# Kernel tuning notes

Hardware: AMD Instinct MI355X
Metric: run time of the kernel (lower is better)

The kernel has to match this reference:

```python
import math
import jax, jax.numpy as jnp
import numpy as np

F0_BINS = 64; FRAME_HOP = 240; SR = 48000; LO_DIM = 16; N_HARM = 32
NOISE_FFT = 256; N_NOISE = NOISE_FFT // 2 + 1; VEL_DIM = 8
F0_MAX = 5000.0; F0_MIN = 20.0
B, T = 4, 500
NSAMP = T * FRAME_HOP
MLP, HID = 128, 64
FEAT = F0_BINS + LO_DIM + VEL_DIM  # 88


def _sincos_enc(norm, dim):
    # norm: (...,) in [0,1] -> (..., dim), even slots sin, odd slots cos
    i = jnp.arange(1, dim // 2 + 1, dtype=jnp.float32)
    ang = math.pi * i * norm[..., None]                    # (..., dim/2)
    return jnp.stack([jnp.sin(ang), jnp.cos(ang)], axis=-1).reshape(norm.shape + (dim,))


def lin_interp(x, out_len):
    # matches F.interpolate(mode='linear', align_corners=False); x: (..., Tin)
    Tin = x.shape[-1]
    pos = jnp.clip((jnp.arange(out_len, dtype=jnp.float32) + 0.5) * (Tin / out_len) - 0.5, 0.0, Tin - 1.0)
    i0 = jnp.floor(pos).astype(jnp.int32)
    i1 = jnp.minimum(i0 + 1, Tin - 1)
    w = pos - i0
    return x[..., i0] * (1.0 - w) + x[..., i1] * w


def _hann(n):
    return 0.5 - 0.5 * jnp.cos(2.0 * math.pi * jnp.arange(n, dtype=jnp.float32) / n)


def _stft(x, n_fft, hop, window):
    # torch.stft with center=True (reflect pad); returns (B, n_fft//2+1, n_frames)
    pad = n_fft // 2
    xp = jnp.pad(x, ((0, 0), (pad, pad)), mode='reflect')
    n_frames = 1 + (xp.shape[-1] - n_fft) // hop
    idx = jnp.arange(n_frames)[:, None] * hop + jnp.arange(n_fft)[None, :]
    frames = xp[:, idx] * window                           # (B, F, n_fft)
    return jnp.swapaxes(jnp.fft.rfft(frames, axis=-1), 1, 2)


def _istft(spec, n_fft, hop, window, length):
    frames = jnp.fft.irfft(jnp.swapaxes(spec, 1, 2), n=n_fft, axis=-1) * window  # (B, F, n_fft)
    nF = frames.shape[1]
    out_len = n_fft + hop * (nF - 1)
    idx = jnp.arange(nF)[:, None] * hop + jnp.arange(n_fft)[None, :]
    ola = jnp.zeros((frames.shape[0], out_len), frames.dtype).at[:, idx].add(frames)
    wsum = jnp.zeros((out_len,), frames.dtype).at[idx].add(jnp.broadcast_to(window ** 2, idx.shape))
    ola = ola / jnp.maximum(wsum, 1e-11)
    pad = n_fft // 2
    return ola[:, pad:pad + length]


def _gru(x, W_ih, W_hh, b_ih, b_hh):
    # torch nn.GRU, 1 layer, batch_first; gates ordered (r, z, n)
    H = W_hh.shape[1]
    def step(h, xt):
        gi = xt @ W_ih.T + b_ih
        gh = h @ W_hh.T + b_hh
        ir, iz, inn = jnp.split(gi, 3, axis=-1)
        hr, hz, hn = jnp.split(gh, 3, axis=-1)
        r = jax.nn.sigmoid(ir + hr)
        z = jax.nn.sigmoid(iz + hz)
        n = jnp.tanh(inn + r * hn)
        h_new = (1.0 - z) * n + z * h
        return h_new, h_new
    h0 = jnp.zeros((x.shape[0], H), x.dtype)
    _, ys = jax.lax.scan(step, h0, jnp.swapaxes(x, 0, 1))
    return jnp.swapaxes(ys, 0, 1)


def _harm_synth(harm_amps, overall_amp, f0_hz, n_samples):
    Bn, Tf, N = harm_amps.shape
    a = lin_interp(jnp.swapaxes(harm_amps, 1, 2), n_samples)      # (B, N, n)
    oa = lin_interp(jnp.swapaxes(overall_amp, 1, 2), n_samples)   # (B, 1, n)
    f0_up = lin_interp(f0_hz, n_samples)                          # (B, n)
    k = jnp.arange(1, N + 1, dtype=jnp.float32)
    inst_freq = f0_up[:, None, :] * k[None, :, None]              # (B, N, n)
    a = a * (inst_freq < SR * 0.45).astype(a.dtype)
    mean_freq = inst_freq.mean(axis=2, keepdims=True)             # (B, N, 1) -- faithful to source
    t = jnp.arange(n_samples, dtype=jnp.float32)
    phase = (2.0 * math.pi / SR) * mean_freq * t[None, None, :]
    return (a * jnp.sin(phase)).sum(axis=1, keepdims=True) * oa   # (B, 1, n)


def _noise_synth(noise_mags, noise, n_samples, n_fft=NOISE_FFT):
    hop = n_fft // 4
    window = _hann(n_fft)
    spec = _stft(noise, n_fft, hop, window)                       # (B, 129, T_stft)
    T_stft = spec.shape[-1]
    mag = lin_interp(jnp.swapaxes(noise_mags, 1, 2), T_stft)      # (B, 129, T_stft)
    return _istft(spec * mag, n_fft, hop, window, n_samples)[:, None, :]


def setup_inputs() -> dict:
    key = jax.random.key(0)
    ks = jax.random.split(key, 20)
    def lin(k, o, i, s=0.05):
        return jax.random.normal(k, (o, i), dtype=jnp.float32) * s
    inp = {
        'f0_hz': jax.random.uniform(ks[0], (B, T), jnp.float32) * 1980.0 + 20.0,
        'loudness_db': jax.random.uniform(ks[1], (B, T), jnp.float32) * -80.0,
        'velocity': jax.random.uniform(ks[2], (B,), jnp.float32) * 7.0,
        'noise_L': jax.random.normal(ks[3], (B, NSAMP), jnp.float32),
        'noise_R': jax.random.normal(ks[4], (B, NSAMP), jnp.float32),
        'W_pre1': lin(ks[5], MLP, FEAT), 'b_pre1': jnp.zeros((MLP,), jnp.float32),
        'W_pre2': lin(ks[6], MLP, MLP), 'b_pre2': jnp.zeros((MLP,), jnp.float32),
        'W_ih': lin(ks[7], 3 * HID, MLP), 'W_hh': lin(ks[8], 3 * HID, HID),
        'b_ih': jnp.zeros((3 * HID,), jnp.float32), 'b_hh': jnp.zeros((3 * HID,), jnp.float32),
        'W_post': lin(ks[9], MLP, HID), 'b_post': jnp.zeros((MLP,), jnp.float32),
        'W_hL': lin(ks[10], N_HARM, MLP), 'b_hL': jnp.zeros((N_HARM,), jnp.float32),
        'W_hR': lin(ks[11], N_HARM, MLP), 'b_hR': jnp.zeros((N_HARM,), jnp.float32),
        'W_amp': lin(ks[12], 1, MLP), 'b_amp': jnp.zeros((1,), jnp.float32),
        'W_nL': lin(ks[13], N_NOISE, MLP), 'b_nL': jnp.full((N_NOISE,), -3.0, jnp.float32),
        'W_nR': lin(ks[14], N_NOISE, MLP), 'b_nR': jnp.full((N_NOISE,), -3.0, jnp.float32),
    }
    return inp


def reference(f0_hz, loudness_db, velocity, noise_L, noise_R,
              W_pre1, b_pre1, W_pre2, b_pre2,
              W_ih, W_hh, b_ih, b_hh, W_post, b_post,
              W_hL, b_hL, W_hR, b_hR, W_amp, b_amp,
              W_nL, b_nL, W_nR, b_nR):
    Bn, Tn = f0_hz.shape
    # --- sinusoidal encodings ---
    f0_safe = jnp.clip(f0_hz, F0_MIN, None)
    f0_norm = jnp.clip((jnp.log(f0_safe) - math.log(F0_MIN)) / (math.log(F0_MAX) - math.log(F0_MIN)), 0.0, 1.0)
    f0_enc = _sincos_enc(f0_norm, F0_BINS) * (f0_hz > 0).astype(jnp.float32)[..., None]
    lo_enc = _sincos_enc(jnp.clip((loudness_db + 80.0) / 80.0, 0.0, 1.0), LO_DIM)
    vel_enc = _sincos_enc(jnp.clip(velocity / 7.0, 0.0, 1.0), VEL_DIM)  # (B, VEL_DIM)
    vel_enc = jnp.broadcast_to(vel_enc[:, None, :], (Bn, Tn, VEL_DIM))
    feat = jnp.concatenate([f0_enc, lo_enc, vel_enc], axis=-1)          # (B, T, 88)
    # --- trunk ---
    feat = jax.nn.relu(feat @ W_pre1.T + b_pre1)
    feat = jax.nn.relu(feat @ W_pre2.T + b_pre2)
    feat = _gru(feat, W_ih, W_hh, b_ih, b_hh)
    feat = jax.nn.relu(feat @ W_post.T + b_post)
    # --- heads ---
    harm_L = jax.nn.sigmoid(feat @ W_hL.T + b_hL)
    harm_R = jax.nn.sigmoid(feat @ W_hR.T + b_hR)
    overall_amp = jax.nn.softplus(feat @ W_amp.T + b_amp)               # (B, T, 1)
    nmag_L = jax.nn.sigmoid(feat @ W_nL.T + b_nL)
    nmag_R = jax.nn.sigmoid(feat @ W_nR.T + b_nR)
    n_samples = Tn * FRAME_HOP
    # --- synthesis ---
    L = _harm_synth(harm_L, overall_amp, f0_hz, n_samples) + _noise_synth(nmag_L, noise_L, n_samples)
    R = _harm_synth(harm_R, overall_amp, f0_hz, n_samples) + _noise_synth(nmag_R, noise_R, n_samples)
    return jnp.concatenate([L, R], axis=1)                              # (B, 2, n_samples)
```

## Files before the change

### kernel.cpp

```cpp
#include <hip/hip_runtime.h>
#include <math.h>

#ifndef M_PI
#define M_PI 3.14159265358979323846
#endif

#define BB 4
#define TT 500
#define NSAMP 120000
#define NHARM 32
#define NFFT 256
#define NBIN 129
#define NHOPF 64
#define NFRAMES 1876
#define HID 64
#define MLPD 128
#define FEATD 88

#define R_MAG ((float)(500.0/1876.0))
#define R_UP_F ((float)(500.0/120000.0))

#define OFF_HARML 0
#define OFF_HARMR 64000
#define OFF_AMP   128000
#define OFF_NMAGL 130000
#define OFF_NMAGR 388000
#define OFF_C1    646000
#define OFF_H1    646128
#define OFF_GI    (OFF_H1+256000)
#define OFF_GOUT  (OFF_GI+384000)
#define OFF_SPECL (OFF_GOUT+128000)
#define OFF_SPECR (OFF_SPECL+4*NFRAMES*258)

__device__ __forceinline__ void up_coords(int m, int* i0, int* i1, float* w, float* w1){
  float pos = __fadd_rn(__fmul_rn(__fadd_rn((float)m, 0.5f), R_UP_F), -0.5f);
  pos = fminf(fmaxf(pos, 0.0f), 499.0f);
  int a = (int)pos;
  *i0 = a; *i1 = min(a+1, TT-1);
  float ww = __fsub_rn(pos, (float)a);
  *w = ww; *w1 = __fsub_rn(1.0f, ww);
}
__device__ __forceinline__ float f0_up_elem(const float* __restrict__ f0s, int m){
  int i0,i1; float w,w1;
  up_coords(m,&i0,&i1,&w,&w1);
  return __fadd_rn(__fmul_rn(f0s[i0], w1), __fmul_rn(f0s[i1], w));
}

__global__ __launch_bounds__(128) void k_encmm(const float* __restrict__ f0,
    const float* __restrict__ ldb, const float* __restrict__ vel,
    const float* __restrict__ Wp1, const float* __restrict__ bp1,
    float* __restrict__ h1){
  int row = blockIdx.x;
  int b = row / TT;
  int tid = threadIdx.x;
  __shared__ float feat[FEATD];
  if (tid < FEATD){
    float f = f0[row];
    float gate = (f > 0.0f) ? 1.0f : 0.0f;
    float fs = fmaxf(f, 20.0f);
    float fn = (logf(fs) - (float)2.995732273553991) / (float)5.5214609178622464;
    fn = fminf(fmaxf(fn, 0.0f), 1.0f);
    float ln = fminf(fmaxf((ldb[row] + 80.0f) / 80.0f, 0.0f), 1.0f);
    float vn = fminf(fmaxf(vel[b] / 7.0f, 0.0f), 1.0f);
    float norm; int i; float g2 = 1.0f;
    if (tid < 64){ i = (tid>>1) + 1; norm = fn; g2 = gate; }
    else if (tid < 80){ i = ((tid-64)>>1) + 1; norm = ln; }
    else { i = ((tid-80)>>1) + 1; norm = vn; }
    float ang = (float)M_PI * (float)i * norm;
    feat[tid] = ((tid & 1) ? cosf(ang) : sinf(ang)) * g2;
  }
  __syncthreads();
  const float* wp = Wp1 + tid*FEATD;
  float acc = bp1[tid];
  #pragma unroll 8
  for (int i=0;i<FEATD;i++) acc = fmaf(feat[i], wp[i], acc);
  h1[(size_t)row*MLPD + tid] = fmaxf(acc, 0.0f);
}

__global__ __launch_bounds__(192) void k_mm2gi(const float* __restrict__ h1,
    const float* __restrict__ Wp2, const float* __restrict__ bp2,
    const float* __restrict__ Wih, const float* __restrict__ bih,
    float* __restrict__ gi){
  int row = blockIdx.x;
  int tid = threadIdx.x;
  __shared__ float h1s[MLPD];
  __shared__ float h2s[MLPD];
  if (tid < MLPD) h1s[tid] = h1[(size_t)row*MLPD + tid];
  __syncthreads();
  if (tid < MLPD){
    const float* wp = Wp2 + tid*MLPD;
    float acc = bp2[tid];
    #pragma unroll 8
    for (int i=0;i<MLPD;i++) acc = fmaf(h1s[i], wp[i], acc);
    h2s[tid] = fmaxf(acc, 0.0f);
  }
  __syncthreads();
  const float* wp = Wih + tid*MLPD;
  float acc = bih[tid];
  #pragma unroll 8
  for (int i=0;i<MLPD;i++) acc = fmaf(h2s[i], wp[i], acc);
  gi[(size_t)row*192 + tid] = acc;
}

__device__ float np_block_sum(const float* __restrict__ f0s, int off, int n, float kf){
  float r[8];
  #pragma unroll
  for (int j=0;j<8;j++) r[j] = __fmul_rn(f0_up_elem(f0s, off+j), kf);
  int lim = n - (n & 7);
  int i = 8;
  for (; i<lim; i+=8){
    #pragma unroll
    for (int j=0;j<8;j++)
      r[j] = __fadd_rn(r[j], __fmul_rn(f0_up_elem(f0s, off+i+j), kf));
  }
  float res = __fadd_rn(__fadd_rn(__fadd_rn(r[0],r[1]), __fadd_rn(r[2],r[3])),
                        __fadd_rn(__fadd_rn(r[4],r[5]), __fadd_rn(r[6],r[7])));
  for (; i<n; i++)
    res = __fadd_rn(res, __fmul_rn(f0_up_elem(f0s, off+i), kf));
  return res;
}

#define MID_GRU   BB
#define MID_MF    (MID_GRU + BB*32)
#define STFT_JOBS (2*BB*NFRAMES)
#define MID_STFT_BLOCKS ((STFT_JOBS+5)/6)
#define MID_BLOCKS (MID_MF + MID_STFT_BLOCKS)

#define RL(x,l) __uint_as_float(__builtin_amdgcn_readlane(__float_as_uint(x), (l)))

#define CH  25
#define NCH 20

__device__ __forceinline__ float fsig(float x){
  return __fdividef(1.0f, 1.0f + __expf(-x));
}
__device__ __forceinline__ float ftanh(float x){
  return fmaf(-2.0f, __fdividef(1.0f, 1.0f + __expf(2.0f*x)), 1.0f);
}

__global__ __launch_bounds__(384) void k_mid(
    const float* __restrict__ gi, const float* __restrict__ Whh,
    const float* __restrict__ bhh, float* __restrict__ gout,
    const float* __restrict__ f0, const float* __restrict__ nL,
    const float* __restrict__ nR, float* __restrict__ ws){
  __shared__ __align__(16) float sh[13696];
  int blk = blockIdx.x;
  int tid = threadIdx.x;

  if (blk < MID_GRU){
    float* gibuf = sh;
    float* hist  = sh + 9600;
    int b = blk;
    int j = tid & 63;
    float wr[64], wz[64], wn[64];
    float br=0.f, bz=0.f, bn=0.f;
    if (tid < 64){
      #pragma unroll
      for (int i=0;i<16;i++){
        float4 a = *(const float4*)(Whh + (size_t)(j)*64     + i*4);
        float4 c = *(const float4*)(Whh + (size_t)(64+j)*64  + i*4);
        float4 d = *(const float4*)(Whh + (size_t)(128+j)*64 + i*4);
        wr[4*i]=a.x; wr[4*i+1]=a.y; wr[4*i+2]=a.z; wr[4*i+3]=a.w;
        wz[4*i]=c.x; wz[4*i+1]=c.y; wz[4*i+2]=c.z; wz[4*i+3]=c.w;
        wn[4*i]=d.x; wn[4*i+1]=d.y; wn[4*i+2]=d.z; wn[4*i+3]=d.w;
      }
      br = bhh[j]; bz = bhh[64+j]; bn = bhh[128+j];
    }
    const float* gbase = gi + (size_t)b*TT*192;
    if (tid >= 64){
      int pt = tid - 64;
      for (int idx = pt; idx < CH*48; idx += 192){
        float4 v = *(const float4*)(gbase + idx*4);
        *(float4*)&gibuf[idx*4] = v;
      }
    }
    __syncthreads();
    float hreg = 0.0f;
    float* op = gout + (size_t)b*TT*64;
    for (int c=0; c<NCH; c++){
      if (tid >= 64){
        if (c+1 < NCH){
          int pt = tid - 64;
          const float* src = gbase + (size_t)(c+1)*CH*192;
          float* dst = &gibuf[((c+1)&1)*4800];
          for (int idx = pt; idx < CH*48; idx += 192){
            float4 v = *(const float4*)(src + idx*4);
            *(float4*)&dst[idx*4] = v;
          }
        }
      } else {
        const float* gch = &gibuf[(c&1)*4800];
        for (int tt=0; tt<CH; tt++){
          int t = c*CH + tt;
          float gr0 = gch[tt*192 + j];
          float gz0 = gch[tt*192 + 64 + j];
          float gn0 = gch[tt*192 + 128 + j];
          float ar0=0.f,ar1=0.f,ar2=0.f,ar3=0.f;
          float az0=0.f,az1=0.f,az2=0.f,az3=0.f;
          float an0=0.f,an1=0.f,an2=0.f,an3=0.f;
          #pragma unroll
          for (int i=0;i<16;i++){
            float h0 = RL(hreg, i), h1v = RL(hreg, 16+i);
            float h2v = RL(hreg, 32+i), h3v = RL(hreg, 48+i);
            ar0 = fmaf(wr[i],    h0,  ar0); ar1 = fmaf(wr[16+i], h1v, ar1);
            ar2 = fmaf(wr[32+i], h2v, ar2); ar3 = fmaf(wr[48+i], h3v, ar3);
            az0 = fmaf(wz[i],    h0,  az0); az1 = fmaf(wz[16+i], h1v, az1);
            az2 = fmaf(wz[32+i], h2v, az2); az3 = fmaf(wz[48+i], h3v, az3);
            an0 = fmaf(wn[i],    h0,  an0); an1 = fmaf(wn[16+i], h1v, an1);
            an2 = fmaf(wn[32+i], h2v, an2); an3 = fmaf(wn[48+i], h3v, an3);
          }
          float ar = __fadd_rn(__fadd_rn(ar0,ar1), __fadd_rn(ar2,ar3));
          float az = __fadd_rn(__fadd_rn(az0,az1), __fadd_rn(az2,az3));
          float an = __fadd_rn(__fadd_rn(an0,an1), __fadd_rn(an2,an3));
          float r = fsig(gr0 + ar + br);
          float z = fsig(gz0 + az + bz);
          float n = ftanh(gn0 + r*(an+bn));
          hreg = (1.0f - z)*n + z*hreg;
          int th = t & 63;
          hist[th*64 + j] = hreg;
          if (th == 63 || t == TT-1){
            int base_t = t - th;
            int per = th + 1;
            int nb = per >> 2;
            float* dst2 = op + base_t*64 + j*per;
            for (int q=0;q<nb;q++){
              float4 v = *(float4*)&hist[j*per + q*4];
              *(float4*)&dst2[q*4] = v;
            }
          }
        }
      }
      __syncthreads();
    }
  } else if (blk < MID_MF){
    int bk = blk - MID_GRU;
    int b = bk >> 5, k = bk & 31;
    float kf = (float)(k+1);
    float* f0s = sh;
    float* red = sh + 512;
    for (int i=tid;i<TT;i+=384) f0s[i] = f0[b*TT+i];
    __syncthreads();
    if (tid < 256){
      float lv[4];
      #pragma unroll
      for (int q=0;q<4;q++){
        int leafIdx = tid*4 + q;
        int off = 0, n = NSAMP;
        #pragma unroll
        for (int lvl=9; lvl>=0; --lvl){
          int n2 = (n>>1); n2 -= (n2 & 7);
          if ((leafIdx >> lvl) & 1){ off += n2; n -= n2; } else { n = n2; }
        }
        lv[q] = np_block_sum(f0s, off, n, kf);
      }
      red[tid] = __fadd_rn(__fadd_rn(lv[0],lv[1]), __fadd_rn(lv[2],lv[3]));
    }
    __syncthreads();
    for (int cnt=256; cnt>1; cnt>>=1){
      int half = cnt>>1;
      float v = 0.0f;
      if (tid < half) v = __fadd_rn(red[2*tid], red[2*tid+1]);
      __syncthreads();
      if (tid < half) red[tid] = v;
      __syncthreads();
    }
    if (tid==0){
      float mf = __fdiv_rn(red[0], 120000.0f);
      float c1 = __fmul_rn((float)(2.0*M_PI/48000.0), mf);
      ws[OFF_C1 + b*32 + k] = c1;
    }
  } else {
    int base = (blk - MID_MF)*6;
    int sub = tid >> 6;
    int j = tid & 63;
    float2* tw = (float2*)sh;
    float* frs = sh + 512 + sub*256;
    if (tid < 256){
      double a = (2.0*M_PI/256.0)*(double)tid;
      tw[tid] = make_float2((float)cos(a), (float)sin(a));
    }
    int jid = base + sub;
    bool act = jid < STFT_JOBS;
    int b=0, f=0; const float* x = nL;
    if (act){
      int ch = jid / (BB*NFRAMES);
      int rem = jid - ch*(BB*NFRAMES);
      b = rem / NFRAMES; f = rem - b*NFRAMES;
      x = (ch ? nR : nL) + (size_t)b*NSAMP;
      for (int n=j;n<256;n+=64){
        double a = (2.0*M_PI/256.0)*(double)n;
        int xi = f*NHOPF + n - 128;
        xi = xi < 0 ? -xi : xi;
        xi = xi >= NSAMP ? 2*(NSAMP-1)-xi : xi;
        float wnd = (float)(0.5 - 0.5*cos(a));
        frs[n] = x[xi]*wnd;
      }
    }
    __syncthreads();
    if (act){
      int ch = jid / (BB*NFRAMES);
      float* spec = ws + (ch ? OFF_SPECR : OFF_SPECL) + (size_t)(b*NFRAMES+f)*258;
      float re0=0.f, im0=0.f, re1=0.f, im1=0.f;
      int m0 = 0;
      #pragma unroll 4
      for (int n=0;n<256;n++){
        float fv = frs[n];
        int m1 = (m0 + ((n&3)<<6)) & 255;
        float2 t0 = tw[m0], t1 = tw[m1];
        re0 = fmaf(fv, t0.x, re0); im0 = fmaf(-fv, t0.y, im0);
        re1 = fmaf(fv, t1.x, re1); im1 = fmaf(-fv, t1.y, im1);
        m0 = (m0 + j) & 255;
      }
      float pq = frs[j] + frs[j+64] + frs[j+128] + frs[j+192];
      pq = (j & 1) ? -pq : pq;
      for (int o2=32;o2>0;o2>>=1) pq += __shfl_down(pq, o2, 64);
      spec[2*j]   = re0; spec[2*j+1]   = im0;
      spec[2*(j+64)] = re1; spec[2*(j+64)+1] = im1;
      if (j==0){ spec[256] = pq; spec[257] = 0.0f; }
    }
  }
}

__global__ __launch_bounds__(128) void k_posthead(const float* __restrict__ gout,
  const float* __restrict__ Wpo, const float* __restrict__ bpo,
  const float* __restrict__ WhL, const float* __restrict__ bhL,
  const float* __restrict__ WhR, const float* __restrict__ bhR,
  const float* __restrict__ Wam, const float* __restrict__ bam,
  const float* __restrict__ WnL, const float* __restrict__ bnL,
  const float* __restrict__ WnR, const float* __restrict__ bnR,
  float* __restrict__ harmL, float* __restrict__ harmR, float* __restrict__ amp,
  float* __restrict__ nmagL, float* __restrict__ nmagR){
  int row = blockIdx.x;
  int tid = threadIdx.x;
  __shared__ float gs[HID];
  __shared__ float post[MLPD];
  if (tid < HID) gs[tid] = gout[(size_t)row*HID + tid];
  __syncthreads();
  {
    const float* wp = Wpo + tid*HID;
    float acc = bpo[tid];
    #pragma unroll 8
    for (int i=0;i<HID;i++) acc = fmaf(gs[i], wp[i], acc);
    post[tid] = fmaxf(acc, 0.0f);
  }
  __syncthreads();
  #pragma unroll
  for (int rr=0;rr<3;rr++){
    int c = tid + rr*128;
    if (c >= 323) break;
    const float* W; const float* bb; float* o; int oc, ow; bool sp=false;
    if (c < 32)      { W=WhL; bb=bhL; o=harmL; oc=c;     ow=32; }
    else if (c < 64) { W=WhR; bb=bhR; o=harmR; oc=c-32;  ow=32; }
    else if (c == 64){ W=Wam; bb=bam; o=amp;   oc=0;     ow=1; sp=true; }
    else if (c < 194){ W=WnL; bb=bnL; o=nmagL; oc=c-65;  ow=129; }
    else             { W=WnR; bb=bnR; o=nmagR; oc=c-194; ow=129; }
    const float* wp = W + oc*MLPD;
    float acc = bb[oc];
    #pragma unroll 8
    for (int i=0;i<MLPD;i++) acc = fmaf(post[i], wp[i], acc);
    float v;
    if (sp) v = fmaxf(acc, 0.0f) + log1pf(expf(-fabsf(acc)));
    else    v = 1.0f/(1.0f+expf(-acc));
    o[(size_t)row*ow + oc] = v;
  }
}

__global__ __launch_bounds__(256) void k_istft(float* __restrict__ ws){
  int fr = blockIdx.x;
  int ch = blockIdx.y;
  int b = fr / NFRAMES, f = fr - b*NFRAMES;
  float* spec = ws + (ch ? OFF_SPECR : OFF_SPECL) + (size_t)fr*258;
  const float* nmag = ws + (ch ? OFF_NMAGR : OFF_NMAGL) + (size_t)b*TT*NBIN;
  int t = threadIdx.x;
  __shared__ float2 mx[NBIN];
  double a = (2.0*M_PI/256.0)*(double)t;
  float cz = (float)cos(a), sz = (float)sin(a);
  if (t < NBIN){
    float pos = ((float)f + 0.5f) * R_MAG - 0.5f;
    pos = fminf(fmaxf(pos, 0.0f), 499.0f);
    int i0 = (int)pos, i1 = min(i0+1, TT-1);
    float w = pos - (float)i0;
    float mg = nmag[i0*NBIN + t]*(1.0f-w) + nmag[i1*NBIN + t]*w;
    mx[t] = make_float2(spec[2*t]*mg, spec[2*t+1]*mg);
  }
  __syncthreads();
  float acc0 = mx[0].x + ((t&1) ? -mx[128].x : mx[128].x);
  float acc = 0.0f;
  float c = cz, s = sz;
  #pragma unroll 4
  for (int k=1;k<128;k++){
    float2 v = mx[k];
    acc = fmaf(v.x, c, acc);
    acc = fmaf(-v.y, s, acc);
    float ts_ = s*sz, tc_ = c*sz;
    float cn = fmaf(c, cz, -ts_);
    float sn = fmaf(s, cz,  tc_);
    c = cn; s = sn;
  }
  float y = (acc0 + 2.0f*acc) * (1.0f/256.0f);
  float win = 0.5f - 0.5f*cz;
  spec[t] = y*win;
}

__global__ __launch_bounds__(256) void k_out(const float* __restrict__ f0,
    const float* __restrict__ ws, float* __restrict__ out){
  __shared__ float win2[256];
  __shared__ float c1s[BB*32];
  {
    int t = threadIdx.x;
    double a = (2.0*M_PI/256.0)*(double)t;
    float w = (float)(0.5 - 0.5*cos(a));
    win2[t] = w*w;
    if (t < BB*32) c1s[t] = ws[OFF_C1 + t];
  }
  __syncthreads();
  int idx = blockIdx.x*256 + threadIdx.x;
  if (idx >= BB*2*NSAMP) return;
  int m = idx % NSAMP;
  int bc = idx / NSAMP;
  int ch = bc & 1, b = bc >> 1;
  int i0,i1; float w,w1;
  up_coords(m,&i0,&i1,&w,&w1);
  const float* f0b = f0 + b*TT;
  float f0u = __fadd_rn(__fmul_rn(f0b[i0], w1), __fmul_rn(f0b[i1], w));
  const float* am = ws + OFF_AMP + b*TT;
  float oa = __fadd_rn(__fmul_rn(am[i0], w1), __fmul_rn(am[i1], w));
  const float* ha = ws + (ch ? OFF_HARMR : OFF_HARML) + (size_t)b*TT*NHARM;
  float tm = (float)m;
  float hsum = 0.0f;
  for (int k=1;k<=NHARM;k++){
    float instf = __fmul_rn(f0u, (float)k);
    if (instf < 21600.0f){
      float a0 = ha[i0*NHARM + (k-1)], a1 = ha[i1*NHARM + (k-1)];
      float ak = __fadd_rn(__fmul_rn(a0, w1), __fmul_rn(a1, w));
      float ph = __fmul_rn(c1s[b*32 + (k-1)], tm);
      double rev = (double)ph * 0.15915494309189535;
      double fr2 = rev - floor(rev);
      float rad = (float)((fr2 - (fr2 >= 0.5 ? 1.0 : 0.0)) * 6.283185307179586);
      float s = sinf(rad);
      hsum = __fadd_rn(hsum, __fmul_rn(ak, s));
    }
  }
  float harm = __fmul_rn(hsum, oa);
  int p = m + 128;
  int fhi = min(p >> 6, NFRAMES-1);
  int flo = max((p - 192) >> 6, 0);
  const float* frb = ws + (ch ? OFF_SPECR : OFF_SPECL) + (size_t)b*NFRAMES*258;
  float nacc = 0.0f, wsum = 0.0f;
  for (int f=flo; f<=fhi; f++){
    int n = p - f*NHOPF;
    nacc += frb[f*258 + n];
    wsum += win2[n];
  }
  float noise = nacc / fmaxf(wsum, 1e-11f);
  out[idx] = __fadd_rn(harm, noise);
}

extern "C" void kernel_launch(void* const* d_in, const int* in_sizes, int n_in,
                              void* d_out, int out_size, void* d_ws, size_t ws_size,
                              hipStream_t stream){
  const float* f0  = (const float*)d_in[0];
  const float* ldb = (const float*)d_in[1];
  const float* vel = (const float*)d_in[2];
  const float* nL  = (const float*)d_in[3];
  const float* nR  = (const float*)d_in[4];
  const float* Wp1 = (const float*)d_in[5];
  const float* bp1 = (const float*)d_in[6];
  const float* Wp2 = (const float*)d_in[7];
  const float* bp2 = (const float*)d_in[8];
  const float* Wih = (const float*)d_in[9];
  const float* Whh = (const float*)d_in[10];
  const float* bih = (const float*)d_in[11];
  const float* bhh = (const float*)d_in[12];
  const float* Wpo = (const float*)d_in[13];
  const float* bpo = (const float*)d_in[14];
  const float* WhL = (const float*)d_in[15];
  const float* bhL = (const float*)d_in[16];
  const float* WhR = (const float*)d_in[17];
  const float* bhR = (const float*)d_in[18];
  const float* Wam = (const float*)d_in[19];
  const float* bam = (const float*)d_in[20];
  const float* WnL = (const float*)d_in[21];
  const float* bnL = (const float*)d_in[22];
  const float* WnR = (const float*)d_in[23];
  const float* bnR = (const float*)d_in[24];
  float* ws = (float*)d_ws;
  float* out = (float*)d_out;

  k_encmm<<<BB*TT, 128, 0, stream>>>(f0, ldb, vel, Wp1, bp1, ws+OFF_H1);
  k_mm2gi<<<BB*TT, 192, 0, stream>>>(ws+OFF_H1, Wp2, bp2, Wih, bih, ws+OFF_GI);
  k_mid<<<MID_BLOCKS, 384, 0, stream>>>(ws+OFF_GI, Whh, bhh, ws+OFF_GOUT, f0, nL, nR, ws);
  k_posthead<<<BB*TT, 128, 0, stream>>>(ws+OFF_GOUT, Wpo, bpo,
      WhL,bhL, WhR,bhR, Wam,bam, WnL,bnL, WnR,bnR,
      ws+OFF_HARML, ws+OFF_HARMR, ws+OFF_AMP, ws+OFF_NMAGL, ws+OFF_NMAGR);
  dim3 gs(BB*NFRAMES, 2);
  k_istft<<<gs, 256, 0, stream>>>(ws);
  k_out<<<(BB*2*NSAMP+255)/256, 256, 0, stream>>>(f0, ws, out);
}
```

Measured before the change: 457.0 us.

## Fuse front MLP kernels and use packed FMA in GRU recurrence

Merges the encoder/first-layer kernel with the second-layer/GRU-input kernel, so h1 stays in shared memory and one launch plus a global round trip are removed. In the serial GRU recurrence inside k_mid, the 64-wide dot products are rewritten with two-element vector FMAs, which can map to packed FP32 FMA on CDNA3-class hardware and halve the FMA issue count on the critical serial path. k_mid also gets an explicit waves-per-EU hint to steer register allocation. The packed form changes the summation order slightly, and the occupancy hint may affect the other roles that share k_mid.

```diff
diff --git a/kernel.cpp b/kernel.cpp
--- a/kernel.cpp
+++ b/kernel.cpp
@@ -20,6 +20,8 @@
 #define R_MAG ((float)(500.0/1876.0))
 #define R_UP_F ((float)(500.0/120000.0))
 
+typedef float v2f __attribute__((ext_vector_type(2)));
+
 #define OFF_HARML 0
 #define OFF_HARMR 64000
 #define OFF_AMP   128000
@@ -46,14 +48,18 @@
   return __fadd_rn(__fmul_rn(f0s[i0], w1), __fmul_rn(f0s[i1], w));
 }
 
-__global__ __launch_bounds__(128) void k_encmm(const float* __restrict__ f0,
+__global__ __launch_bounds__(192) void k_front(const float* __restrict__ f0,
     const float* __restrict__ ldb, const float* __restrict__ vel,
     const float* __restrict__ Wp1, const float* __restrict__ bp1,
-    float* __restrict__ h1){
+    const float* __restrict__ Wp2, const float* __restrict__ bp2,
+    const float* __restrict__ Wih, const float* __restrict__ bih,
+    float* __restrict__ gi){
   int row = blockIdx.x;
   int b = row / TT;
   int tid = threadIdx.x;
   __shared__ float feat[FEATD];
+  __shared__ float h1s[MLPD];
+  __shared__ float h2s[MLPD];
   if (tid < FEATD){
     float f = f0[row];
     float gate = (f > 0.0f) ? 1.0f : 0.0f;
@@ -70,22 +76,13 @@
     feat[tid] = ((tid & 1) ? cosf(ang) : sinf(ang)) * g2;
   }
   __syncthreads();
-  const float* wp = Wp1 + tid*FEATD;
-  float acc = bp1[tid];
-  #pragma unroll 8
-  for (int i=0;i<FEATD;i++) acc = fmaf(feat[i], wp[i], acc);
-  h1[(size_t)row*MLPD + tid] = fmaxf(acc, 0.0f);
-}
-
-__global__ __launch_bounds__(192) void k_mm2gi(const float* __restrict__ h1,
-    const float* __restrict__ Wp2, const float* __restrict__ bp2,
-    const float* __restrict__ Wih, const float* __restrict__ bih,
-    float* __restrict__ gi){
-  int row = blockIdx.x;
-  int tid = threadIdx.x;
-  __shared__ float h1s[MLPD];
-  __shared__ float h2s[MLPD];
-  if (tid < MLPD) h1s[tid] = h1[(size_t)row*MLPD + tid];
+  if (tid < MLPD){
+    const float* wp = Wp1 + tid*FEATD;
+    float acc = bp1[tid];
+    #pragma unroll 8
+    for (int i=0;i<FEATD;i++) acc = fmaf(feat[i], wp[i], acc);
+    h1s[tid] = fmaxf(acc, 0.0f);
+  }
   __syncthreads();
   if (tid < MLPD){
     const float* wp = Wp2 + tid*MLPD;
@@ -95,11 +92,13 @@
     h2s[tid] = fmaxf(acc, 0.0f);
   }
   __syncthreads();
-  const float* wp = Wih + tid*MLPD;
-  float acc = bih[tid];
-  #pragma unroll 8
-  for (int i=0;i<MLPD;i++) acc = fmaf(h2s[i], wp[i], acc);
-  gi[(size_t)row*192 + tid] = acc;
+  {
+    const float* wp = Wih + tid*MLPD;
+    float acc = bih[tid];
+    #pragma unroll 8
+    for (int i=0;i<MLPD;i++) acc = fmaf(h2s[i], wp[i], acc);
+    gi[(size_t)row*192 + tid] = acc;
+  }
 }
 
 __device__ float np_block_sum(const float* __restrict__ f0s, int off, int n, float kf){
@@ -138,7 +137,10 @@
   return fmaf(-2.0f, __fdividef(1.0f, 1.0f + __expf(2.0f*x)), 1.0f);
 }
 
-__global__ __launch_bounds__(384) void k_mid(
+__global__
+__attribute__((amdgpu_flat_work_group_size(384,384)))
+__attribute__((amdgpu_waves_per_eu(2,2)))
+void k_mid(
     const float* __restrict__ gi, const float* __restrict__ Whh,
     const float* __restrict__ bhh, float* __restrict__ gout,
     const float* __restrict__ f0, const float* __restrict__ nL,
@@ -152,7 +154,7 @@
     float* hist  = sh + 9600;
     int b = blk;
     int j = tid & 63;
-    float wr[64], wz[64], wn[64];
+    v2f wr2[32], wz2[32], wn2[32];
     float br=0.f, bz=0.f, bn=0.f;
     if (tid < 64){
       #pragma unroll
@@ -160,9 +162,9 @@
         float4 a = *(const float4*)(Whh + (size_t)(j)*64     + i*4);
         float4 c = *(const float4*)(Whh + (size_t)(64+j)*64  + i*4);
         float4 d = *(const float4*)(Whh + (size_t)(128+j)*64 + i*4);
-        wr[4*i]=a.x; wr[4*i+1]=a.y; wr[4*i+2]=a.z; wr[4*i+3]=a.w;
-        wz[4*i]=c.x; wz[4*i+1]=c.y; wz[4*i+2]=c.z; wz[4*i+3]=c.w;
-        wn[4*i]=d.x; wn[4*i+1]=d.y; wn[4*i+2]=d.z; wn[4*i+3]=d.w;
+        wr2[2*i] = (v2f){a.x, a.y}; wr2[2*i+1] = (v2f){a.z, a.w};
+        wz2[2*i] = (v2f){c.x, c.y}; wz2[2*i+1] = (v2f){c.z, c.w};
+        wn2[2*i] = (v2f){d.x, d.y}; wn2[2*i+1] = (v2f){d.z, d.w};
       }
       br = bhh[j]; bz = bhh[64+j]; bn = bhh[128+j];
     }
@@ -195,23 +197,24 @@
           float gr0 = gch[tt*192 + j];
           float gz0 = gch[tt*192 + 64 + j];
           float gn0 = gch[tt*192 + 128 + j];
-          float ar0=0.f,ar1=0.f,ar2=0.f,ar3=0.f;
-          float az0=0.f,az1=0.f,az2=0.f,az3=0.f;
-          float an0=0.f,an1=0.f,an2=0.f,an3=0.f;
+          v2f AR0={0.f,0.f}, AR1={0.f,0.f};
+          v2f AZ0={0.f,0.f}, AZ1={0.f,0.f};
+          v2f AN0={0.f,0.f}, AN1={0.f,0.f};
           #pragma unroll
           for (int i=0;i<16;i++){
-            float h0 = RL(hreg, i), h1v = RL(hreg, 16+i);
-            float h2v = RL(hreg, 32+i), h3v = RL(hreg, 48+i);
-            ar0 = fmaf(wr[i],    h0,  ar0); ar1 = fmaf(wr[16+i], h1v, ar1);
-            ar2 = fmaf(wr[32+i], h2v, ar2); ar3 = fmaf(wr[48+i], h3v, ar3);
-            az0 = fmaf(wz[i],    h0,  az0); az1 = fmaf(wz[16+i], h1v, az1);
-            az2 = fmaf(wz[32+i], h2v, az2); az3 = fmaf(wz[48+i], h3v, az3);
-            an0 = fmaf(wn[i],    h0,  an0); an1 = fmaf(wn[16+i], h1v, an1);
-            an2 = fmaf(wn[32+i], h2v, an2); an3 = fmaf(wn[48+i], h3v, an3);
+            v2f hA, hB;
+            hA.x = RL(hreg, 2*i);    hA.y = RL(hreg, 2*i+1);
+            hB.x = RL(hreg, 32+2*i); hB.y = RL(hreg, 33+2*i);
+            AR0 = __builtin_elementwise_fma(wr2[i],    hA, AR0);
+            AR1 = __builtin_elementwise_fma(wr2[16+i], hB, AR1);
+            AZ0 = __builtin_elementwise_fma(wz2[i],    hA, AZ0);
+            AZ1 = __builtin_elementwise_fma(wz2[16+i], hB, AZ1);
+            AN0 = __builtin_elementwise_fma(wn2[i],    hA, AN0);
+            AN1 = __builtin_elementwise_fma(wn2[16+i], hB, AN1);
           }
-          float ar = __fadd_rn(__fadd_rn(ar0,ar1), __fadd_rn(ar2,ar3));
-          float az = __fadd_rn(__fadd_rn(az0,az1), __fadd_rn(az2,az3));
-          float an = __fadd_rn(__fadd_rn(an0,an1), __fadd_rn(an2,an3));
+          float ar = __fadd_rn(__fadd_rn(AR0.x,AR0.y), __fadd_rn(AR1.x,AR1.y));
+          float az = __fadd_rn(__fadd_rn(AZ0.x,AZ0.y), __fadd_rn(AZ1.x,AZ1.y));
+          float an = __fadd_rn(__fadd_rn(AN0.x,AN0.y), __fadd_rn(AN1.x,AN1.y));
           float r = fsig(gr0 + ar + br);
           float z = fsig(gz0 + az + bz);
           float n = ftanh(gn0 + r*(an+bn));
@@ -487,8 +490,7 @@
   float* ws = (float*)d_ws;
   float* out = (float*)d_out;
 
-  k_encmm<<<BB*TT, 128, 0, stream>>>(f0, ldb, vel, Wp1, bp1, ws+OFF_H1);
-  k_mm2gi<<<BB*TT, 192, 0, stream>>>(ws+OFF_H1, Wp2, bp2, Wih, bih, ws+OFF_GI);
+  k_front<<<BB*TT, 192, 0, stream>>>(f0, ldb, vel, Wp1, bp1, Wp2, bp2, Wih, bih, ws+OFF_GI);
   k_mid<<<MID_BLOCKS, 384, 0, stream>>>(ws+OFF_GI, Whh, bhh, ws+OFF_GOUT, f0, nL, nR, ws);
   k_posthead<<<BB*TT, 128, 0, stream>>>(ws+OFF_GOUT, Wpo, bpo,
       WhL,bhL, WhR,bhR, Wam,bam, WnL,bnL, WnR,bnR,
```

Measured after the change: 433.1 us. 1.06x faster.
